# Optimization experiments

Measured on AMD Instinct MI355X. Metric: run time of the kernel, lower is better.

## Reference

```python
import jax, jax.numpy as jnp
import numpy as np

IN_FEATURES = 512
NUM_CASES = 64
N_POINTS = 131072
HIDDEN = 512
OUT_FEATURES = 512


def _wn_linear(x, V, g, b):
    # torch weight_norm with dim=0 on Linear weight [out, in]: per-row norm over in-dim
    W = V * (g / jnp.linalg.norm(V, axis=1))[:, None]
    return x @ W.T + b


def _consolidative_matmul(mask, x):
    # group-by-caseID mean pooling expressed as masked matmul (matches torch forward)
    sel_sum = jnp.sum(mask, axis=-1, keepdims=True)
    sel_sum = jnp.maximum(sel_sum, 1.0)  # relu(s-1)+1 == max(s,1) for s>=0
    return (mask @ x) / sel_sum


def setup_inputs() -> dict:
    key = jax.random.key(0)
    ks = jax.random.split(key, 8)
    feat = jax.random.normal(ks[0], (N_POINTS, IN_FEATURES), dtype=jnp.float32)
    cid = jax.random.randint(ks[1], (N_POINTS, 1), 0, NUM_CASES).astype(jnp.float32)
    x = jnp.concatenate([feat, cid], axis=-1)  # [N, 513]
    s = 0.05
    V0 = jax.random.normal(ks[2], (HIDDEN, IN_FEATURES), dtype=jnp.float32) * s
    g0 = jnp.ones((HIDDEN,), dtype=jnp.float32)
    b0 = jnp.zeros((HIDDEN,), dtype=jnp.float32)
    V1 = jax.random.normal(ks[3], (HIDDEN, HIDDEN), dtype=jnp.float32) * s
    g1 = jnp.ones((HIDDEN,), dtype=jnp.float32)
    b1 = jnp.zeros((HIDDEN,), dtype=jnp.float32)
    Wf = jax.random.normal(ks[4], (OUT_FEATURES, HIDDEN), dtype=jnp.float32) * s
    bf = jnp.zeros((OUT_FEATURES,), dtype=jnp.float32)
    return {"x": x, "V0": V0, "g0": g0, "b0": b0,
            "V1": V1, "g1": g1, "b1": b1, "Wf": Wf, "bf": bf}


def reference(x, V0, g0, b0, V1, g1, b1, Wf, bf):
    feat = x[..., :IN_FEATURES]                    # [N, 512]
    cid = jax.lax.stop_gradient(x[..., IN_FEATURES:IN_FEATURES + 1])  # [N, 1]
    case_range = jnp.arange(NUM_CASES, dtype=x.dtype)[:, None]        # [C, 1]
    d = jnp.swapaxes(cid, -1, -2) - case_range     # [C, N]
    # Unit_function: 1 iff -0.5 < d < 0.5, else 0 (hard, zero-grad)
    mask = jnp.where((d > -0.5) & (d < 0.5), 1.0, 0.0).astype(x.dtype)
    mask = jax.lax.stop_gradient(mask)
    h = _consolidative_matmul(mask, feat)          # [C, 512] per-case mean
    h = jax.nn.silu(_wn_linear(h, V0, g0, b0))
    h = jax.nn.silu(_wn_linear(h, V1, g1, b1))
    h = h @ Wf.T + bf                              # final layer, identity activation
    out = jnp.swapaxes(mask, -1, -2) @ h           # scatter-back combine [N, 512]
    return out
```

## Files before the change

### kernel.cpp

```cpp
#include <hip/hip_runtime.h>
#include <math.h>

#define NPTS   131072
#define INF    512
#define ROWF   513
#define NCASE  64
#define HID    512
#define NB     256
#define CHUNK  512
#define SEG    32

__global__ __launch_bounds__(256)
void k_hist(const float* __restrict__ x, int* __restrict__ hist,
            int* __restrict__ cids) {
  __shared__ int h[NCASE];
  const int t = threadIdx.x;
  const int b = blockIdx.x;
  if (t < NCASE) h[t] = 0;
  __syncthreads();
  const int base = b * CHUNK;
  for (int i = t; i < CHUNK; i += 256) {
    float cf = x[(size_t)(base + i) * ROWF + INF];
    int c = (int)(cf + 0.5f);
    cids[base + i] = c;
    atomicAdd(&h[c], 1);
  }
  __syncthreads();
  if (t < NCASE) hist[t * NB + b] = h[t];
}

__global__ __launch_bounds__(256)
void k_scan(const int* __restrict__ hist, int* __restrict__ rel,
            int* __restrict__ cnt) {
  __shared__ int buf[NB];
  const int c = blockIdx.x;
  const int t = threadIdx.x;
  const int v = hist[c * NB + t];
  buf[t] = v;
  __syncthreads();
  for (int d = 1; d < NB; d <<= 1) {
    int u = (t >= d) ? buf[t - d] : 0;
    __syncthreads();
    buf[t] += u;
    __syncthreads();
  }
  rel[t * NCASE + c] = buf[t] - v;
  if (t == NB - 1) cnt[c] = buf[t];
}

__global__ __launch_bounds__(64)
void k_build(const int* __restrict__ cids, const int* __restrict__ rel,
             const int* __restrict__ cnt, int* __restrict__ idxlist) {
  __shared__ int cidl[CHUNK];
  const int lane = threadIdx.x;
  const int b = blockIdx.x;
  for (int i = lane; i < CHUNK; i += 64) cidl[i] = cids[b * CHUNK + i];
  int lv = cnt[lane];
  int sc = lv;
  for (int d = 1; d < 64; d <<= 1) {
    int u = __shfl_up(sc, d, 64);
    if (lane >= d) sc += u;
  }
  const int base = sc - lv;
  __syncthreads();
  int myoff = rel[b * NCASE + lane] + base;
  int rank = 0;
  for (int i = 0; i < CHUNK; ++i) {
    if (cidl[i] == lane) { idxlist[myoff + rank] = b * CHUNK + i; ++rank; }
  }
}

__global__ __launch_bounds__(128)
void k_sum(const float* __restrict__ x, const int* __restrict__ idxlist,
           const int* __restrict__ cnt, float* __restrict__ psum) {
  const int t = threadIdx.x;
  const int s = blockIdx.x;
  const int c = blockIdx.y;
  const int lane = t & 63;

  int lv = cnt[lane];
  int sc = lv;
  for (int d = 1; d < 64; d <<= 1) {
    int u = __shfl_up(sc, d, 64);
    if (lane >= d) sc += u;
  }
  const int bs = __shfl(sc - lv, c, 64);
  const int n  = __shfl(lv, c, 64);

  int p0 = (s * n) / SEG;
  int p1 = ((s + 1) * n) / SEG;

  float a0 = 0.f, a1 = 0.f, a2 = 0.f, a3 = 0.f;
  int p = p0;
  for (; p + 8 <= p1; p += 8) {
    int idx[8];
    #pragma unroll
    for (int j = 0; j < 8; ++j)
      idx[j] = __builtin_amdgcn_readfirstlane(idxlist[bs + p + j]);
    float v[8][4];
    #pragma unroll
    for (int j = 0; j < 8; ++j) {
      const float* r = x + (size_t)idx[j] * ROWF + t;
      v[j][0] = r[0]; v[j][1] = r[128]; v[j][2] = r[256]; v[j][3] = r[384];
    }
    #pragma unroll
    for (int j = 0; j < 8; ++j) {
      a0 += v[j][0]; a1 += v[j][1]; a2 += v[j][2]; a3 += v[j][3];
    }
  }
  for (; p < p1; ++p) {
    int i0 = __builtin_amdgcn_readfirstlane(idxlist[bs + p]);
    const float* r = x + (size_t)i0 * ROWF + t;
    a0 += r[0]; a1 += r[128]; a2 += r[256]; a3 += r[384];
  }
  float* od = psum + ((size_t)c * SEG + s) * HID;
  od[t] = a0; od[t + 128] = a1; od[t + 256] = a2; od[t + 384] = a3;
}

__global__ __launch_bounds__(256)
void k_scale2(const float* __restrict__ V0, const float* __restrict__ g0,
              const float* __restrict__ V1, const float* __restrict__ g1,
              float* __restrict__ scale0, float* __restrict__ scale1) {
  __shared__ float red[256];
  const int row = blockIdx.x;
  const int t   = threadIdx.x;
  const bool first = row < 512;
  const int r = first ? row : row - 512;
  const float* vr = (first ? V0 : V1) + (size_t)r * HID;
  float s = 0.f;
  for (int k = t; k < HID; k += 256) { float v = vr[k]; s += v * v; }
  red[t] = s;
  __syncthreads();
  for (int w = 128; w > 0; w >>= 1) {
    if (t < w) red[t] += red[t + w];
    __syncthreads();
  }
  if (t == 0) {
    float g = first ? g0[r] : g1[r];
    (first ? scale0 : scale1)[r] = g / sqrtf(red[0]);
  }
}

template <bool SILU, bool SCALED, bool REDUCE>
__global__ __launch_bounds__(256)
void k_layer(const float* __restrict__ hin, const float* __restrict__ W,
             const float* __restrict__ scale, const float* __restrict__ bias,
             const int* __restrict__ cnt, float* __restrict__ hout) {
  __shared__ float hrow[HID];
  const int n = blockIdx.y;
  const int t = threadIdx.x;
  const int o = blockIdx.x * 256 + t;
  if (REDUCE) {
    float inv = 1.f / fmaxf((float)cnt[n], 1.f);
    for (int f = t; f < HID; f += 256) {
      float s = 0.f;
      for (int seg = 0; seg < SEG; ++seg)
        s += hin[((size_t)n * SEG + seg) * HID + f];
      hrow[f] = s * inv;
    }
  } else {
    for (int f = t; f < HID; f += 256) hrow[f] = hin[(size_t)n * HID + f];
  }
  __syncthreads();
  const float* wr = W + (size_t)o * HID;
  float s0 = 0.f, s1 = 0.f, s2 = 0.f, s3 = 0.f;
  for (int k = 0; k < HID; k += 4) {
    float4 h4 = *(const float4*)&hrow[k];
    float4 w4 = *(const float4*)&wr[k];
    s0 += h4.x * w4.x; s1 += h4.y * w4.y;
    s2 += h4.z * w4.z; s3 += h4.w * w4.w;
  }
  float sdot = (s0 + s1) + (s2 + s3);
  float y = SCALED ? (sdot * scale[o] + bias[o]) : (sdot + bias[o]);
  if (SILU) y = y / (1.f + expf(-y));
  hout[(size_t)n * HID + o] = y;
}

__global__ __launch_bounds__(256)
void k_scatter(const int* __restrict__ cids, const float* __restrict__ h3,
               float* __restrict__ out) {
  __shared__ int cl[64];
  const int t = threadIdx.x;
  const int q = t & 127;
  const int half = t >> 7;
  const int base = blockIdx.x * 64;
  if (t < 64) cl[t] = cids[base + t];
  __syncthreads();
  #pragma unroll 4
  for (int p = half; p < 64; p += 2) {
    int c = cl[p];
    float4 hv = ((const float4*)(h3 + (size_t)c * HID))[q];
    ((float4*)(out + (size_t)(base + p) * HID))[q] = hv;
  }
}

extern "C" void kernel_launch(void* const* d_in, const int* in_sizes, int n_in,
                              void* d_out, int out_size, void* d_ws, size_t ws_size,
                              hipStream_t stream) {
  const float* x  = (const float*)d_in[0];
  const float* V0 = (const float*)d_in[1];
  const float* g0 = (const float*)d_in[2];
  const float* b0 = (const float*)d_in[3];
  const float* V1 = (const float*)d_in[4];
  const float* g1 = (const float*)d_in[5];
  const float* b1 = (const float*)d_in[6];
  const float* Wf = (const float*)d_in[7];
  const float* bf = (const float*)d_in[8];
  float* out = (float*)d_out;
  float* ws  = (float*)d_ws;

  size_t off = 0;
  float* psum   = ws + off; off += (size_t)NCASE * SEG * HID;
  float* h1     = ws + off; off += NCASE * HID;
  float* h2     = ws + off; off += NCASE * HID;
  float* h3     = ws + off; off += NCASE * HID;
  float* scale0 = ws + off; off += 512;
  float* scale1 = ws + off; off += 512;
  int* iws = (int*)(ws + off);
  size_t ioff = 0;
  int* hist    = iws + ioff; ioff += NCASE * NB;
  int* rel     = iws + ioff; ioff += NB * NCASE;
  int* cnt     = iws + ioff; ioff += NCASE;
  int* cids    = iws + ioff; ioff += NPTS;
  int* idxlist = iws + ioff; ioff += NPTS;

  k_scale2<<<dim3(1024), dim3(256), 0, stream>>>(V0, g0, V1, g1, scale0, scale1);
  k_hist  <<<dim3(NB), dim3(256), 0, stream>>>(x, hist, cids);
  k_scan  <<<dim3(NCASE), dim3(NB), 0, stream>>>(hist, rel, cnt);
  k_build <<<dim3(NB), dim3(64), 0, stream>>>(cids, rel, cnt, idxlist);
  k_sum   <<<dim3(SEG, NCASE), dim3(128), 0, stream>>>(x, idxlist, cnt, psum);
  k_layer<true,  true,  true ><<<dim3(2, NCASE), dim3(256), 0, stream>>>(psum, V0, scale0, b0, cnt, h1);
  k_layer<true,  true,  false><<<dim3(2, NCASE), dim3(256), 0, stream>>>(h1,   V1, scale1, b1, cnt, h2);
  k_layer<false, false, false><<<dim3(2, NCASE), dim3(256), 0, stream>>>(h2,   Wf, nullptr, bf, cnt, h3);
  k_scatter<<<dim3(NPTS / 64), dim3(256), 0, stream>>>(cids, h3, out);
}
```

Measured before the change: 233.2 us.

## Restructure gather-sum with per-wave row split and nontemporal loads/stores

The segmented gather-sum now assigns each of two wavefronts its own subset of rows. Each lane covers 8 strided features, row indices are loaded cooperatively and broadcast with shuffles, and the two wave partials are combined through shared memory. The number of segments per case is halved, so there are fewer partial sums to reduce. Reads of x and writes of the output use nontemporal hints, and the scatter kernel handles 128 points per block. The aim is more memory-level parallelism and less cache pollution from streaming data, at the cost of fewer blocks in the sum kernel.

```diff
diff --git a/kernel.cpp b/kernel.cpp
--- a/kernel.cpp
+++ b/kernel.cpp
@@ -8,7 +8,9 @@
 #define HID    512
 #define NB     256
 #define CHUNK  512
-#define SEG    32
+#define SEG    16
+
+typedef float v4f __attribute__((ext_vector_type(4)));
 
 __global__ __launch_bounds__(256)
 void k_hist(const float* __restrict__ x, int* __restrict__ hist,
@@ -73,10 +75,12 @@
 __global__ __launch_bounds__(128)
 void k_sum(const float* __restrict__ x, const int* __restrict__ idxlist,
            const int* __restrict__ cnt, float* __restrict__ psum) {
-  const int t = threadIdx.x;
+  __shared__ float buf[2][HID];
+  const int t = threadIdx.x;
+  const int lane = t & 63;
+  const int w = t >> 6;
   const int s = blockIdx.x;
   const int c = blockIdx.y;
-  const int lane = t & 63;
 
   int lv = cnt[lane];
   int sc = lv;
@@ -87,34 +91,46 @@
   const int bs = __shfl(sc - lv, c, 64);
   const int n  = __shfl(lv, c, 64);
 
-  int p0 = (s * n) / SEG;
-  int p1 = ((s + 1) * n) / SEG;
-
-  float a0 = 0.f, a1 = 0.f, a2 = 0.f, a3 = 0.f;
-  int p = p0;
-  for (; p + 8 <= p1; p += 8) {
-    int idx[8];
-    #pragma unroll
-    for (int j = 0; j < 8; ++j)
-      idx[j] = __builtin_amdgcn_readfirstlane(idxlist[bs + p + j]);
-    float v[8][4];
-    #pragma unroll
-    for (int j = 0; j < 8; ++j) {
-      const float* r = x + (size_t)idx[j] * ROWF + t;
-      v[j][0] = r[0]; v[j][1] = r[128]; v[j][2] = r[256]; v[j][3] = r[384];
+  const int p0 = (s * n) / SEG;
+  const int p1 = ((s + 1) * n) / SEG;
+  const int m  = p1 - p0;
+
+  float a[8];
+  #pragma unroll
+  for (int k = 0; k < 8; ++k) a[k] = 0.f;
+
+  for (int j0 = w * 64; j0 < m; j0 += 128) {
+    const int nb = (m - j0 < 64) ? (m - j0) : 64;
+    int iv = (lane < nb) ? idxlist[bs + p0 + j0 + lane] : 0;
+    int jj = 0;
+    for (; jj + 4 <= nb; jj += 4) {
+      float v[4][8];
+      #pragma unroll
+      for (int u = 0; u < 4; ++u) {
+        int idx = __shfl(iv, jj + u, 64);
+        const float* r = x + (size_t)idx * ROWF + lane;
+        #pragma unroll
+        for (int k = 0; k < 8; ++k) v[u][k] = __builtin_nontemporal_load(r + 64 * k);
+      }
+      #pragma unroll
+      for (int u = 0; u < 4; ++u) {
+        #pragma unroll
+        for (int k = 0; k < 8; ++k) a[k] += v[u][k];
+      }
     }
-    #pragma unroll
-    for (int j = 0; j < 8; ++j) {
-      a0 += v[j][0]; a1 += v[j][1]; a2 += v[j][2]; a3 += v[j][3];
+    for (; jj < nb; ++jj) {
+      int idx = __shfl(iv, jj, 64);
+      const float* r = x + (size_t)idx * ROWF + lane;
+      #pragma unroll
+      for (int k = 0; k < 8; ++k) a[k] += __builtin_nontemporal_load(r + 64 * k);
     }
   }
-  for (; p < p1; ++p) {
-    int i0 = __builtin_amdgcn_readfirstlane(idxlist[bs + p]);
-    const float* r = x + (size_t)i0 * ROWF + t;
-    a0 += r[0]; a1 += r[128]; a2 += r[256]; a3 += r[384];
-  }
+
+  #pragma unroll
+  for (int k = 0; k < 8; ++k) buf[w][lane + 64 * k] = a[k];
+  __syncthreads();
   float* od = psum + ((size_t)c * SEG + s) * HID;
-  od[t] = a0; od[t + 128] = a1; od[t + 256] = a2; od[t + 384] = a3;
+  for (int f = t; f < HID; f += 128) od[f] = buf[0][f] + buf[1][f];
 }
 
 __global__ __launch_bounds__(256)
@@ -179,18 +195,19 @@
 __global__ __launch_bounds__(256)
 void k_scatter(const int* __restrict__ cids, const float* __restrict__ h3,
                float* __restrict__ out) {
-  __shared__ int cl[64];
+  __shared__ int cl[128];
   const int t = threadIdx.x;
   const int q = t & 127;
   const int half = t >> 7;
-  const int base = blockIdx.x * 64;
-  if (t < 64) cl[t] = cids[base + t];
-  __syncthreads();
-  #pragma unroll 4
-  for (int p = half; p < 64; p += 2) {
+  const int base = blockIdx.x * 128;
+  if (t < 128) cl[t] = cids[base + t];
+  __syncthreads();
+  #pragma unroll 8
+  for (int p = half; p < 128; p += 2) {
     int c = cl[p];
-    float4 hv = ((const float4*)(h3 + (size_t)c * HID))[q];
-    ((float4*)(out + (size_t)(base + p) * HID))[q] = hv;
+    v4f hv = ((const v4f*)(h3 + (size_t)c * HID))[q];
+    v4f* dst = (v4f*)(out + (size_t)(base + p) * HID) + q;
+    __builtin_nontemporal_store(hv, dst);
   }
 }
 
@@ -232,5 +249,5 @@
   k_layer<true,  true,  true ><<<dim3(2, NCASE), dim3(256), 0, stream>>>(psum, V0, scale0, b0, cnt, h1);
   k_layer<true,  true,  false><<<dim3(2, NCASE), dim3(256), 0, stream>>>(h1,   V1, scale1, b1, cnt, h2);
   k_layer<false, false, false><<<dim3(2, NCASE), dim3(256), 0, stream>>>(h2,   Wf, nullptr, bf, cnt, h3);
-  k_scatter<<<dim3(NPTS / 64), dim3(256), 0, stream>>>(cids, h3, out);
-}
+  k_scatter<<<dim3(NPTS / 128), dim3(256), 0, stream>>>(cids, h3, out);
+}
```

New measurement: 200.0 us. -14.2%, faster.
